# Kernel tuning notes

Measured on AMD Instinct MI355X. Metric: run time of the kernel, lower is better.

The kernel has to match this reference:

```python
import jax, jax.numpy as jnp
import numpy as np

B, T, D, H = 2, 2048, 2048, 32
HD = D // H
# quantization scales (constructor-time attributes in the original repo)
A_PROJ = 3e-4   # q/k/v proj alpha (W8A8B8O8Linear)
A_QK = 2e-5     # qk_bmm alpha (BMM_S8T_S8N_F32T)
A_PV = 1e-2     # pv_bmm alpha (BMM_S8T_S8N_S8T)
A_OUT = 1e-4    # out_proj alpha (W8A8BFP32OFP32Linear)


def _i8(key, shape):
    return jax.random.randint(key, shape, -128, 128, dtype=jnp.int32).astype(jnp.int8)


def setup_inputs() -> dict:
    key = jax.random.key(0)
    ks = jax.random.split(key, 10)
    hidden_states = _i8(ks[0], (B, T, D))
    # causal mask, 0 on/below diagonal, large negative above
    causal = jnp.triu(jnp.full((T, T), -1e9, dtype=jnp.float32), k=1)
    attention_mask = jnp.broadcast_to(causal, (B, 1, T, T))
    return {
        "hidden_states": hidden_states,
        "attention_mask": attention_mask,
        "Wq": _i8(ks[1], (D, D)), "bq": _i8(ks[2], (D,)),
        "Wk": _i8(ks[3], (D, D)), "bk": _i8(ks[4], (D,)),
        "Wv": _i8(ks[5], (D, D)), "bv": _i8(ks[6], (D,)),
        "Wo": _i8(ks[7], (D, D)),
        "bo": jax.random.normal(ks[8], (D,), dtype=jnp.float32),
    }


def _w8a8b8o8(x_i8, W_i8, b_i8, alpha):
    # int8 GEMM -> int32 accum; epilogue: alpha*acc + bias, saturate to int8
    acc = jnp.einsum('btk,nk->btn', x_i8.astype(jnp.int32), W_i8.astype(jnp.int32))
    y = alpha * acc.astype(jnp.float32) + b_i8.astype(jnp.float32)
    return jnp.clip(jnp.round(y), -128, 127).astype(jnp.int8)


def reference(hidden_states, attention_mask, Wq, bq, Wk, bk, Wv, bv, Wo, bo):
    # q/k/v projections: int8 in, int8 out
    q = _w8a8b8o8(hidden_states, Wq, bq, A_PROJ)
    k = _w8a8b8o8(hidden_states, Wk, bk, A_PROJ)
    v = _w8a8b8o8(hidden_states, Wv, bv, A_PROJ)

    def shape(x):  # [B,T,D] -> [B,H,T,HD]
        return x.reshape(B, T, H, HD).transpose(0, 2, 1, 3)

    qh, kh, vh = shape(q), shape(k), shape(v)

    # qk_bmm (BMM_S8T_S8N_F32T): fp32 = alpha * int8 q @ k^T
    attn = A_QK * jnp.einsum('bhtd,bhsd->bhts',
                             qh.astype(jnp.int32), kh.astype(jnp.int32)).astype(jnp.float32)
    attn = attn + attention_mask  # [B,1,T,T] broadcasts over heads
    attn = jnp.maximum(attn, jnp.finfo(jnp.float32).min)
    probs = jax.nn.softmax(attn, axis=-1)

    # quantize probs: p.mul_(127).round_() -> int8
    p_i8 = jnp.clip(jnp.round(probs * 127.0), -128, 127).astype(jnp.int8)

    # pv_bmm (BMM_S8T_S8N_S8T): int8 out = sat(round(alpha * p @ v))
    pv = jnp.einsum('bhts,bhsd->bhtd', p_i8.astype(jnp.int32), vh.astype(jnp.int32))
    attn_out_i8 = jnp.clip(jnp.round(A_PV * pv.astype(jnp.float32)), -128, 127).astype(jnp.int8)

    # [B,H,T,HD] -> [B,T,D]
    attn_out = attn_out_i8.transpose(0, 2, 1, 3).reshape(B, T, D)

    # out_proj (W8A8BFP32OFP32Linear): fp32 = alpha*(x@W^T) + fp32 bias
    acc = jnp.einsum('btk,nk->btn', attn_out.astype(jnp.int32), Wo.astype(jnp.int32))
    out = A_OUT * acc.astype(jnp.float32) + bo
    return out
```

## Files before the change

### kernel.cpp

```cpp
#include <hip/hip_runtime.h>
#include <cstdint>

#define A_PROJ 3e-4f
#define A_QK   2e-5f
#define A_PV   1e-2f
#define A_OUT  1e-4f

#define NB 2
#define NT 2048
#define ND 2048
#define NH 32
#define NHD 64
#define NM (NB*NT)

typedef int v4i __attribute__((ext_vector_type(4)));

__device__ __forceinline__ int8_t sat8(float y) {
  float r = rintf(y);
  r = fminf(fmaxf(r, -128.f), 127.f);
  return (int8_t)(int)r;
}

__device__ __forceinline__ float exp2_fast(float x) {
  return __builtin_amdgcn_exp2f(x);
}

__device__ __forceinline__ void gl2lds16(const int8_t* g, int8_t* l) {
  __builtin_amdgcn_global_load_lds(
      (const __attribute__((address_space(1))) void*)g,
      (__attribute__((address_space(3))) void*)l, 16, 0, 0);
}

#define NWW (ND*ND/4)
__global__ void pack_all(const int* __restrict__ X,
                         const int* __restrict__ W0, const int* __restrict__ W1,
                         const int* __restrict__ W2, const int* __restrict__ W3,
                         int8_t* __restrict__ dX, int8_t* __restrict__ dW0,
                         int8_t* __restrict__ dW1, int8_t* __restrict__ dW2,
                         int8_t* __restrict__ dW3) {
  int i = blockIdx.x * blockDim.x + threadIdx.x;
  const int nx = NM*ND/4;
  const int* src; int8_t* dst; int off;
  if (i < nx) { src = X; dst = dX; off = i; }
  else {
    int j = i - nx;
    int r = j >> 20;
    off = j & (NWW - 1);
    src = (r == 0) ? W0 : (r == 1) ? W1 : (r == 2) ? W2 : W3;
    dst = (r == 0) ? dW0 : (r == 1) ? dW1 : (r == 2) ? dW2 : dW3;
  }
  int4 v = ((const int4*)src)[off];
  uint32_t p = (uint32_t)(v.x & 255) | ((uint32_t)(v.y & 255) << 8) |
               ((uint32_t)(v.z & 255) << 16) | ((uint32_t)(v.w & 255) << 24);
  ((uint32_t*)dst)[off] = p;
}

__global__ __launch_bounds__(256) void gemm_qkv(
    const int8_t* __restrict__ X,
    const int8_t* __restrict__ Wq, const int8_t* __restrict__ Wk, const int8_t* __restrict__ Wv,
    const int* __restrict__ bq, const int* __restrict__ bk, const int* __restrict__ bv,
    int8_t* __restrict__ Qh, int8_t* __restrict__ Kh, int8_t* __restrict__ Vt)
{
  __shared__ __align__(16) int8_t As[2][128][64];
  __shared__ __align__(16) int8_t Bs[2][128][64];
  const int z = blockIdx.z;
  const int8_t* W  = (z == 0) ? Wq : ((z == 1) ? Wk : Wv);
  const int* bias  = (z == 0) ? bq : ((z == 1) ? bk : bv);
  const int m0 = blockIdx.x * 128, n0 = blockIdx.y * 128;
  const int tid = threadIdx.x, lane = tid & 63, wave = tid >> 6;
  const int wm = wave >> 1, wn = wave & 1;
  const int l15 = lane & 15, quad = lane >> 4;

  const int srow = lane >> 2;
  const int scol = (((lane & 3) ^ ((lane >> 3) & 3)) * 16);
  const int rqcol = (quad ^ ((l15 >> 1) & 3)) * 16;

  v4i acc[4][4];
  const v4i vzero = {0, 0, 0, 0};
  #pragma unroll
  for (int i = 0; i < 4; ++i)
    #pragma unroll
    for (int j = 0; j < 4; ++j) acc[i][j] = vzero;

  for (int k0 = 0; k0 < ND; k0 += 128) {
    #pragma unroll
    for (int j = 0; j < 8; ++j) {
      int slot = j * 4 + wave;
      int sl = slot & 15;
      int hh = sl >> 3, rblk = sl & 7;
      int row = rblk * 16 + srow;
      if (slot < 16) {
        gl2lds16(&X[(size_t)(m0 + row) * ND + k0 + hh * 64 + scol], &As[hh][rblk * 16][0]);
      } else {
        gl2lds16(&W[(size_t)(n0 + row) * ND + k0 + hh * 64 + scol], &Bs[hh][rblk * 16][0]);
      }
    }
    __syncthreads();
    #pragma unroll
    for (int hh = 0; hh < 2; ++hh) {
      v4i a[4], b[4];
      #pragma unroll
      for (int mt = 0; mt < 4; ++mt) a[mt] = *(const v4i*)&As[hh][wm*64 + mt*16 + l15][rqcol];
      #pragma unroll
      for (int nt = 0; nt < 4; ++nt) b[nt] = *(const v4i*)&Bs[hh][wn*64 + nt*16 + l15][rqcol];
      #pragma unroll
      for (int mt = 0; mt < 4; ++mt)
        #pragma unroll
        for (int nt = 0; nt < 4; ++nt)
          acc[mt][nt] = __builtin_amdgcn_mfma_i32_16x16x64_i8(a[mt], b[nt], acc[mt][nt], 0, 0, 0);
    }
    __syncthreads();
  }

  float bf[4];
  #pragma unroll
  for (int nt = 0; nt < 4; ++nt) bf[nt] = (float)bias[n0 + wn*64 + nt*16 + l15];

  if (z == 2) {
    #pragma unroll
    for (int mt = 0; mt < 4; ++mt)
      #pragma unroll
      for (int nt = 0; nt < 4; ++nt) {
        int tbase = (m0 + wm*64 + mt*16 + quad*4) & (NT - 1);
        int bb = (m0 + wm*64) >> 11;
        int n = n0 + wn*64 + nt*16 + l15;
        int hh = n >> 6, hd = n & (NHD - 1);
        uint32_t pk = 0;
        #pragma unroll
        for (int r = 0; r < 4; ++r) {
          uint32_t q = (uint32_t)(uint8_t)sat8(A_PROJ * (float)acc[mt][nt][r] + bf[nt]);
          pk |= q << (8 * r);
        }
        size_t bh = (size_t)bb * NH + hh;
        *(uint32_t*)&Vt[(bh * NHD + hd) * NT + tbase] = pk;
      }
  } else {
    int8_t* O = (z == 0) ? Qh : Kh;
    #pragma unroll
    for (int mt = 0; mt < 4; ++mt)
      #pragma unroll
      for (int nt = 0; nt < 4; ++nt)
        #pragma unroll
        for (int r = 0; r < 4; ++r) {
          int m = m0 + wm*64 + mt*16 + quad*4 + r;
          int n = n0 + wn*64 + nt*16 + l15;
          int8_t q = sat8(A_PROJ * (float)acc[mt][nt][r] + bf[nt]);
          int bb = m >> 11, t = m & (NT - 1);
          int hh = n >> 6, hd = n & (NHD - 1);
          size_t bh = (size_t)bb * NH + hh;
          O[(bh * NT + t) * NHD + hd] = q;
        }
  }
}

__global__ __launch_bounds__(256) void attn_fused(
    const int8_t* __restrict__ Qh, const int8_t* __restrict__ Kh, const int8_t* __restrict__ Vt,
    int8_t* __restrict__ AO)
{
  __shared__ __align__(16) int8_t Ks[128][64];
  __shared__ __align__(16) int8_t Vs[64][128];
  __shared__ __align__(16) uint32_t Ps32[4][16][36];

  const int bx = blockIdx.x;
  const int bh = blockIdx.y;
  const int tid = threadIdx.x, lane = tid & 63, wave = tid >> 6;
  const int l15 = lane & 15, quad = lane >> 4;
  const v4i vzero = {0, 0, 0, 0};
  const float MAGIC = 12582912.0f;
  const float C2 = 2.8853900817779268e-05f;

  const int8_t* Qp = Qh + (size_t)bh * NT * NHD;
  const int8_t* Kp = Kh + (size_t)bh * NT * NHD;
  const int8_t* Vp = Vt + (size_t)bh * NHD * NT;
  const int bb = bh >> 5, hhead = bh & (NH - 1);

  const int kst_row = lane >> 2;
  const int kst_col = (((lane & 3) ^ ((lane >> 3) & 3)) * 16);
  const int vst_row = lane >> 3;
  const int vst_col = (((lane & 7) ^ ((lane >> 3) & 7)) * 16);
  const int kfcol = (quad ^ ((l15 >> 1) & 3)) * 16;

  for (int half = 0; half < 2; ++half) {
    const int xq = half ? (31 - bx) : bx;
    const int t0 = xq * 64;
    const int sd = xq >> 1;
    const int tme = t0 + wave * 16 + l15;

    v4i qf = *(const v4i*)&Qp[(size_t)(t0 + wave * 16 + l15) * NHD + quad * 16];

    float lsum = 0.f;
    for (int st = 0; st <= sd; ++st) {
      const int s0 = st * 128;
      #pragma unroll
      for (int j = 0; j < 2; ++j)
        gl2lds16(&Kp[(size_t)(s0 + j*64 + wave*16 + kst_row) * NHD + kst_col],
                 &Ks[j*64 + wave*16][0]);
      __syncthreads();
      v4i kf[8];
      #pragma unroll
      for (int mt = 0; mt < 8; ++mt) kf[mt] = *(const v4i*)&Ks[mt*16 + l15][kfcol];
      if (st < sd) {
        #pragma unroll
        for (int mt = 0; mt < 8; ++mt) {
          v4i sa = __builtin_amdgcn_mfma_i32_16x16x64_i8(kf[mt], qf, vzero, 0, 0, 0);
          #pragma unroll
          for (int r = 0; r < 4; ++r) lsum += exp2_fast(C2 * (float)sa[r]);
        }
      } else {
        #pragma unroll
        for (int mt = 0; mt < 8; ++mt) {
          v4i sa = __builtin_amdgcn_mfma_i32_16x16x64_i8(kf[mt], qf, vzero, 0, 0, 0);
          const int sbase = s0 + mt*16 + quad*4;
          #pragma unroll
          for (int r = 0; r < 4; ++r) {
            float e = exp2_fast(C2 * (float)sa[r]);
            lsum += (sbase + r <= tme) ? e : 0.f;
          }
        }
      }
      __syncthreads();
    }
    {
      lsum += __shfl_xor(lsum, 16, 64);
      lsum += __shfl_xor(lsum, 32, 64);
    }
    const float linv = 127.0f / lsum;

    v4i accv[4];
    #pragma unroll
    for (int j = 0; j < 4; ++j) accv[j] = vzero;

    for (int st = 0; st <= sd; ++st) {
      const int s0 = st * 128;
      #pragma unroll
      for (int j = 0; j < 2; ++j)
        gl2lds16(&Kp[(size_t)(s0 + j*64 + wave*16 + kst_row) * NHD + kst_col],
                 &Ks[j*64 + wave*16][0]);
      #pragma unroll
      for (int j = 0; j < 2; ++j)
        gl2lds16(&Vp[(size_t)(j*32 + wave*8 + vst_row) * NT + s0 + vst_col],
                 &Vs[j*32 + wave*8][0]);
      __syncthreads();
      v4i kf[8];
      #pragma unroll
      for (int mt = 0; mt < 8; ++mt) kf[mt] = *(const v4i*)&Ks[mt*16 + l15][kfcol];

      if (st < sd) {
        #pragma unroll
        for (int mt = 0; mt < 8; ++mt) {
          v4i sa = __builtin_amdgcn_mfma_i32_16x16x64_i8(kf[mt], qf, vzero, 0, 0, 0);
          uint32_t pk = 0;
          #pragma unroll
          for (int r = 0; r < 4; ++r) {
            float e = exp2_fast(C2 * (float)sa[r]);
            float f = fmaf(e, linv, MAGIC);
            pk |= (__float_as_uint(f) & 0xFFu) << (8 * r);
          }
          Ps32[wave][l15][mt*4 + quad] = pk;
        }
      } else {
        #pragma unroll
        for (int mt = 0; mt < 8; ++mt) {
          v4i sa = __builtin_amdgcn_mfma_i32_16x16x64_i8(kf[mt], qf, vzero, 0, 0, 0);
          uint32_t pk = 0;
          const int sbase = s0 + mt*16 + quad*4;
          #pragma unroll
          for (int r = 0; r < 4; ++r) {
            float e = (sbase + r <= tme) ? exp2_fast(C2 * (float)sa[r]) : 0.f;
            float f = fmaf(e, linv, MAGIC);
            pk |= (__float_as_uint(f) & 0xFFu) << (8 * r);
          }
          Ps32[wave][l15][mt*4 + quad] = pk;
        }
      }
      #pragma unroll
      for (int ks = 0; ks < 2; ++ks) {
        v4i ap = *(const v4i*)&Ps32[wave][l15][ks*16 + quad*4];
        #pragma unroll
        for (int nt2 = 0; nt2 < 4; ++nt2) {
          v4i bv = *(const v4i*)&Vs[nt2*16 + l15][(((ks*4 + quad) ^ (l15 & 7)) * 16)];
          accv[nt2] = __builtin_amdgcn_mfma_i32_16x16x64_i8(ap, bv, accv[nt2], 0, 0, 0);
        }
      }
      __syncthreads();
    }

    #pragma unroll
    for (int nt2 = 0; nt2 < 4; ++nt2)
      #pragma unroll
      for (int r = 0; r < 4; ++r) {
        int t = t0 + wave*16 + quad*4 + r;
        int d = nt2*16 + l15;
        AO[((size_t)bb * NT + t) * ND + hhead * NHD + d] = sat8(A_PV * (float)accv[nt2][r]);
      }
  }
}

__global__ __launch_bounds__(256) void gemm_out(
    const int8_t* __restrict__ X, const int8_t* __restrict__ W,
    const float* __restrict__ bo, float* __restrict__ out)
{
  __shared__ __align__(16) int8_t As[2][128][64];
  __shared__ __align__(16) int8_t Bs[2][128][64];
  const int m0 = blockIdx.x * 128, n0 = blockIdx.y * 128;
  const int tid = threadIdx.x, lane = tid & 63, wave = tid >> 6;
  const int wm = wave >> 1, wn = wave & 1;
  const int l15 = lane & 15, quad = lane >> 4;
  const int srow = lane >> 2;
  const int scol = (((lane & 3) ^ ((lane >> 3) & 3)) * 16);
  const int rqcol = (quad ^ ((l15 >> 1) & 3)) * 16;

  v4i acc[4][4];
  const v4i vzero = {0, 0, 0, 0};
  #pragma unroll
  for (int i = 0; i < 4; ++i)
    #pragma unroll
    for (int j = 0; j < 4; ++j) acc[i][j] = vzero;

  for (int k0 = 0; k0 < ND; k0 += 128) {
    #pragma unroll
    for (int j = 0; j < 8; ++j) {
      int slot = j * 4 + wave;
      int sl = slot & 15;
      int hh = sl >> 3, rblk = sl & 7;
      int row = rblk * 16 + srow;
      if (slot < 16) {
        gl2lds16(&X[(size_t)(m0 + row) * ND + k0 + hh * 64 + scol], &As[hh][rblk * 16][0]);
      } else {
        gl2lds16(&W[(size_t)(n0 + row) * ND + k0 + hh * 64 + scol], &Bs[hh][rblk * 16][0]);
      }
    }
    __syncthreads();
    #pragma unroll
    for (int hh = 0; hh < 2; ++hh) {
      v4i a[4], b[4];
      #pragma unroll
      for (int mt = 0; mt < 4; ++mt) a[mt] = *(const v4i*)&As[hh][wm*64 + mt*16 + l15][rqcol];
      #pragma unroll
      for (int nt = 0; nt < 4; ++nt) b[nt] = *(const v4i*)&Bs[hh][wn*64 + nt*16 + l15][rqcol];
      #pragma unroll
      for (int mt = 0; mt < 4; ++mt)
        #pragma unroll
        for (int nt = 0; nt < 4; ++nt)
          acc[mt][nt] = __builtin_amdgcn_mfma_i32_16x16x64_i8(a[mt], b[nt], acc[mt][nt], 0, 0, 0);
    }
    __syncthreads();
  }

  float bf[4];
  #pragma unroll
  for (int nt = 0; nt < 4; ++nt) bf[nt] = bo[n0 + wn*64 + nt*16 + l15];

  #pragma unroll
  for (int mt = 0; mt < 4; ++mt)
    #pragma unroll
    for (int nt = 0; nt < 4; ++nt)
      #pragma unroll
      for (int r = 0; r < 4; ++r) {
        int m = m0 + wm*64 + mt*16 + quad*4 + r;
        int n = n0 + wn*64 + nt*16 + l15;
        out[(size_t)m * ND + n] = A_OUT * (float)acc[mt][nt][r] + bf[nt];
      }
}

extern "C" void kernel_launch(void* const* d_in, const int* in_sizes, int n_in,
                              void* d_out, int out_size, void* d_ws, size_t ws_size,
                              hipStream_t stream)
{
  const int*   hs  = (const int*)d_in[0];
  const int*   Wq  = (const int*)d_in[2];
  const int*   bq  = (const int*)d_in[3];
  const int*   Wk  = (const int*)d_in[4];
  const int*   bkb = (const int*)d_in[5];
  const int*   Wv  = (const int*)d_in[6];
  const int*   bvb = (const int*)d_in[7];
  const int*   Wo  = (const int*)d_in[8];
  const float* bo  = (const float*)d_in[9];
  float* out = (float*)d_out;

  char* ws = (char*)d_ws;
  const size_t SZ_X = (size_t)NM * ND;
  const size_t SZ_W = (size_t)ND * ND;
  const size_t SZ_H = (size_t)NB * NH * NT * NHD;
  int8_t* Xp  = (int8_t*)ws;
  int8_t* Wqp = (int8_t*)(ws + SZ_X);
  int8_t* Wkp = Wqp + SZ_W;
  int8_t* Wvp = Wkp + SZ_W;
  int8_t* Wop = Wvp + SZ_W;
  int8_t* Qh  = Wop + SZ_W;
  int8_t* Kh  = Qh + SZ_H;
  int8_t* Vt  = Kh + SZ_H;
  int8_t* AO  = Xp;

  const int ntot = (int)(SZ_X/4 + 4 * (SZ_W/4));
  pack_all<<<(ntot + 255) / 256, 256, 0, stream>>>(hs, Wq, Wk, Wv, Wo,
                                                   Xp, Wqp, Wkp, Wvp, Wop);

  gemm_qkv<<<dim3(NM/128, ND/128, 3), 256, 0, stream>>>(Xp, Wqp, Wkp, Wvp, bq, bkb, bvb, Qh, Kh, Vt);
  attn_fused<<<dim3(16, NB*NH), 256, 0, stream>>>(Qh, Kh, Vt, AO);
  gemm_out<<<dim3(NM/128, ND/128), 256, 0, stream>>>(AO, Wop, bo, out);
}
```

Measured before the change: 328.7 us.

## Double-buffer LDS loads in GEMMs and attention, skip masked causal tiles

Both int8 GEMMs move from single-stage 128-wide K tiles to a double-buffered 64-wide K pipeline, so the next tile's global-to-LDS load overlaps the current MFMA work. The attention kernel double-buffers its K tiles the same way, reads V fragments straight from global memory into registers instead of staging them in LDS, and on the diagonal tile skips MFMA/exp work for 16-row subtiles that are fully masked. It also splits the row-sum accumulator into four partial sums and packs the probability bytes with perm instructions. The costs are extra LDS for the second buffer, uncoalesced direct global V loads, and a smaller K step per barrier in the GEMMs.

```diff
diff --git a/kernel.cpp b/kernel.cpp
--- a/kernel.cpp
+++ b/kernel.cpp
@@ -75,6 +75,11 @@
   const int scol = (((lane & 3) ^ ((lane >> 3) & 3)) * 16);
   const int rqcol = (quad ^ ((l15 >> 1) & 3)) * 16;
 
+  const int8_t* Xs0 = X + (size_t)(m0 + wave * 32 + srow) * ND + scol;
+  const int8_t* Xs1 = X + (size_t)(m0 + wave * 32 + 16 + srow) * ND + scol;
+  const int8_t* Ws0 = W + (size_t)(n0 + wave * 32 + srow) * ND + scol;
+  const int8_t* Ws1 = W + (size_t)(n0 + wave * 32 + 16 + srow) * ND + scol;
+
   v4i acc[4][4];
   const v4i vzero = {0, 0, 0, 0};
   #pragma unroll
@@ -82,33 +87,31 @@
     #pragma unroll
     for (int j = 0; j < 4; ++j) acc[i][j] = vzero;
 
-  for (int k0 = 0; k0 < ND; k0 += 128) {
-    #pragma unroll
-    for (int j = 0; j < 8; ++j) {
-      int slot = j * 4 + wave;
-      int sl = slot & 15;
-      int hh = sl >> 3, rblk = sl & 7;
-      int row = rblk * 16 + srow;
-      if (slot < 16) {
-        gl2lds16(&X[(size_t)(m0 + row) * ND + k0 + hh * 64 + scol], &As[hh][rblk * 16][0]);
-      } else {
-        gl2lds16(&W[(size_t)(n0 + row) * ND + k0 + hh * 64 + scol], &Bs[hh][rblk * 16][0]);
-      }
+  gl2lds16(Xs0, &As[0][wave * 32][0]);
+  gl2lds16(Xs1, &As[0][wave * 32 + 16][0]);
+  gl2lds16(Ws0, &Bs[0][wave * 32][0]);
+  gl2lds16(Ws1, &Bs[0][wave * 32 + 16][0]);
+  __syncthreads();
+
+  for (int h = 0; h < 32; ++h) {
+    const int buf = h & 1;
+    if (h < 31) {
+      const int off = (h + 1) * 64;
+      gl2lds16(Xs0 + off, &As[buf ^ 1][wave * 32][0]);
+      gl2lds16(Xs1 + off, &As[buf ^ 1][wave * 32 + 16][0]);
+      gl2lds16(Ws0 + off, &Bs[buf ^ 1][wave * 32][0]);
+      gl2lds16(Ws1 + off, &Bs[buf ^ 1][wave * 32 + 16][0]);
     }
-    __syncthreads();
-    #pragma unroll
-    for (int hh = 0; hh < 2; ++hh) {
-      v4i a[4], b[4];
-      #pragma unroll
-      for (int mt = 0; mt < 4; ++mt) a[mt] = *(const v4i*)&As[hh][wm*64 + mt*16 + l15][rqcol];
-      #pragma unroll
-      for (int nt = 0; nt < 4; ++nt) b[nt] = *(const v4i*)&Bs[hh][wn*64 + nt*16 + l15][rqcol];
-      #pragma unroll
-      for (int mt = 0; mt < 4; ++mt)
-        #pragma unroll
-        for (int nt = 0; nt < 4; ++nt)
-          acc[mt][nt] = __builtin_amdgcn_mfma_i32_16x16x64_i8(a[mt], b[nt], acc[mt][nt], 0, 0, 0);
-    }
+    v4i a[4], b[4];
+    #pragma unroll
+    for (int mt = 0; mt < 4; ++mt) a[mt] = *(const v4i*)&As[buf][wm*64 + mt*16 + l15][rqcol];
+    #pragma unroll
+    for (int nt = 0; nt < 4; ++nt) b[nt] = *(const v4i*)&Bs[buf][wn*64 + nt*16 + l15][rqcol];
+    #pragma unroll
+    for (int mt = 0; mt < 4; ++mt)
+      #pragma unroll
+      for (int nt = 0; nt < 4; ++nt)
+        acc[mt][nt] = __builtin_amdgcn_mfma_i32_16x16x64_i8(a[mt], b[nt], acc[mt][nt], 0, 0, 0);
     __syncthreads();
   }
 
@@ -157,8 +160,7 @@
     const int8_t* __restrict__ Qh, const int8_t* __restrict__ Kh, const int8_t* __restrict__ Vt,
     int8_t* __restrict__ AO)
 {
-  __shared__ __align__(16) int8_t Ks[128][64];
-  __shared__ __align__(16) int8_t Vs[64][128];
+  __shared__ __align__(16) int8_t Ks[2][128][64];
   __shared__ __align__(16) uint32_t Ps32[4][16][36];
 
   const int bx = blockIdx.x;
@@ -176,8 +178,6 @@
 
   const int kst_row = lane >> 2;
   const int kst_col = (((lane & 3) ^ ((lane >> 3) & 3)) * 16);
-  const int vst_row = lane >> 3;
-  const int vst_col = (((lane & 7) ^ ((lane >> 3) & 7)) * 16);
   const int kfcol = (quad ^ ((l15 >> 1) & 3)) * 16;
 
   for (int half = 0; half < 2; ++half) {
@@ -185,102 +185,123 @@
     const int t0 = xq * 64;
     const int sd = xq >> 1;
     const int tme = t0 + wave * 16 + l15;
+    const int mtd = ((xq & 1) << 2) + wave;
 
     v4i qf = *(const v4i*)&Qp[(size_t)(t0 + wave * 16 + l15) * NHD + quad * 16];
 
-    float lsum = 0.f;
+    gl2lds16(&Kp[(size_t)(wave*16 + kst_row) * NHD + kst_col], &Ks[0][wave*16][0]);
+    gl2lds16(&Kp[(size_t)(64 + wave*16 + kst_row) * NHD + kst_col], &Ks[0][64 + wave*16][0]);
+    __syncthreads();
+
+    float lac[4] = {0.f, 0.f, 0.f, 0.f};
     for (int st = 0; st <= sd; ++st) {
-      const int s0 = st * 128;
-      #pragma unroll
-      for (int j = 0; j < 2; ++j)
-        gl2lds16(&Kp[(size_t)(s0 + j*64 + wave*16 + kst_row) * NHD + kst_col],
-                 &Ks[j*64 + wave*16][0]);
-      __syncthreads();
-      v4i kf[8];
-      #pragma unroll
-      for (int mt = 0; mt < 8; ++mt) kf[mt] = *(const v4i*)&Ks[mt*16 + l15][kfcol];
+      const int buf = st & 1;
       if (st < sd) {
+        const size_t s1 = (size_t)(st + 1) * 128;
+        gl2lds16(&Kp[(s1 + wave*16 + kst_row) * NHD + kst_col], &Ks[buf^1][wave*16][0]);
+        gl2lds16(&Kp[(s1 + 64 + wave*16 + kst_row) * NHD + kst_col], &Ks[buf^1][64 + wave*16][0]);
+      }
+      if (st < sd) {
         #pragma unroll
         for (int mt = 0; mt < 8; ++mt) {
-          v4i sa = __builtin_amdgcn_mfma_i32_16x16x64_i8(kf[mt], qf, vzero, 0, 0, 0);
+          v4i kf = *(const v4i*)&Ks[buf][mt*16 + l15][kfcol];
+          v4i sa = __builtin_amdgcn_mfma_i32_16x16x64_i8(kf, qf, vzero, 0, 0, 0);
           #pragma unroll
-          for (int r = 0; r < 4; ++r) lsum += exp2_fast(C2 * (float)sa[r]);
+          for (int r = 0; r < 4; ++r) lac[r] += exp2_fast(C2 * (float)sa[r]);
         }
       } else {
-        #pragma unroll
-        for (int mt = 0; mt < 8; ++mt) {
-          v4i sa = __builtin_amdgcn_mfma_i32_16x16x64_i8(kf[mt], qf, vzero, 0, 0, 0);
-          const int sbase = s0 + mt*16 + quad*4;
-          #pragma unroll
-          for (int r = 0; r < 4; ++r) {
-            float e = exp2_fast(C2 * (float)sa[r]);
-            lsum += (sbase + r <= tme) ? e : 0.f;
+        const int s0 = st * 128;
+        for (int mt = 0; mt <= mtd; ++mt) {
+          v4i kf = *(const v4i*)&Ks[buf][mt*16 + l15][kfcol];
+          v4i sa = __builtin_amdgcn_mfma_i32_16x16x64_i8(kf, qf, vzero, 0, 0, 0);
+          if (mt < mtd) {
+            #pragma unroll
+            for (int r = 0; r < 4; ++r) lac[r] += exp2_fast(C2 * (float)sa[r]);
+          } else {
+            const int sbase = s0 + mt*16 + quad*4;
+            #pragma unroll
+            for (int r = 0; r < 4; ++r) {
+              float e = exp2_fast(C2 * (float)sa[r]);
+              lac[r] += (sbase + r <= tme) ? e : 0.f;
+            }
           }
         }
       }
       __syncthreads();
     }
-    {
-      lsum += __shfl_xor(lsum, 16, 64);
-      lsum += __shfl_xor(lsum, 32, 64);
-    }
+    float lsum = (lac[0] + lac[1]) + (lac[2] + lac[3]);
+    lsum += __shfl_xor(lsum, 16, 64);
+    lsum += __shfl_xor(lsum, 32, 64);
     const float linv = 127.0f / lsum;
 
+    gl2lds16(&Kp[(size_t)(wave*16 + kst_row) * NHD + kst_col], &Ks[0][wave*16][0]);
+    gl2lds16(&Kp[(size_t)(64 + wave*16 + kst_row) * NHD + kst_col], &Ks[0][64 + wave*16][0]);
+    __syncthreads();
+
     v4i accv[4];
     #pragma unroll
     for (int j = 0; j < 4; ++j) accv[j] = vzero;
 
     for (int st = 0; st <= sd; ++st) {
+      const int buf = st & 1;
       const int s0 = st * 128;
-      #pragma unroll
-      for (int j = 0; j < 2; ++j)
-        gl2lds16(&Kp[(size_t)(s0 + j*64 + wave*16 + kst_row) * NHD + kst_col],
-                 &Ks[j*64 + wave*16][0]);
-      #pragma unroll
-      for (int j = 0; j < 2; ++j)
-        gl2lds16(&Vp[(size_t)(j*32 + wave*8 + vst_row) * NT + s0 + vst_col],
-                 &Vs[j*32 + wave*8][0]);
-      __syncthreads();
-      v4i kf[8];
-      #pragma unroll
-      for (int mt = 0; mt < 8; ++mt) kf[mt] = *(const v4i*)&Ks[mt*16 + l15][kfcol];
-
       if (st < sd) {
+        const size_t s1 = (size_t)(st + 1) * 128;
+        gl2lds16(&Kp[(s1 + wave*16 + kst_row) * NHD + kst_col], &Ks[buf^1][wave*16][0]);
+        gl2lds16(&Kp[(s1 + 64 + wave*16 + kst_row) * NHD + kst_col], &Ks[buf^1][64 + wave*16][0]);
+      }
+      v4i bv[8];
+      #pragma unroll
+      for (int ks = 0; ks < 2; ++ks)
+        #pragma unroll
+        for (int nt = 0; nt < 4; ++nt)
+          bv[ks*4 + nt] = *(const v4i*)&Vp[(size_t)(nt*16 + l15) * NT + s0 + ks*64 + quad*16];
+
+      if (st < sd) {
         #pragma unroll
         for (int mt = 0; mt < 8; ++mt) {
-          v4i sa = __builtin_amdgcn_mfma_i32_16x16x64_i8(kf[mt], qf, vzero, 0, 0, 0);
-          uint32_t pk = 0;
-          #pragma unroll
-          for (int r = 0; r < 4; ++r) {
-            float e = exp2_fast(C2 * (float)sa[r]);
-            float f = fmaf(e, linv, MAGIC);
-            pk |= (__float_as_uint(f) & 0xFFu) << (8 * r);
+          v4i kf = *(const v4i*)&Ks[buf][mt*16 + l15][kfcol];
+          v4i sa = __builtin_amdgcn_mfma_i32_16x16x64_i8(kf, qf, vzero, 0, 0, 0);
+          uint32_t f0 = __float_as_uint(fmaf(exp2_fast(C2 * (float)sa[0]), linv, MAGIC));
+          uint32_t f1 = __float_as_uint(fmaf(exp2_fast(C2 * (float)sa[1]), linv, MAGIC));
+          uint32_t f2 = __float_as_uint(fmaf(exp2_fast(C2 * (float)sa[2]), linv, MAGIC));
+          uint32_t f3 = __float_as_uint(fmaf(exp2_fast(C2 * (float)sa[3]), linv, MAGIC));
+          uint32_t lo = __builtin_amdgcn_perm(f1, f0, 0x00000400u);
+          uint32_t hi = __builtin_amdgcn_perm(f3, f2, 0x00000400u);
+          Ps32[wave][l15][mt*4 + quad] = __builtin_amdgcn_perm(hi, lo, 0x05040100u);
+        }
+      } else {
+        for (int mt = 0; mt <= mtd; ++mt) {
+          v4i kf = *(const v4i*)&Ks[buf][mt*16 + l15][kfcol];
+          v4i sa = __builtin_amdgcn_mfma_i32_16x16x64_i8(kf, qf, vzero, 0, 0, 0);
+          float e0, e1, e2, e3;
+          if (mt < mtd) {
+            e0 = exp2_fast(C2 * (float)sa[0]); e1 = exp2_fast(C2 * (float)sa[1]);
+            e2 = exp2_fast(C2 * (float)sa[2]); e3 = exp2_fast(C2 * (float)sa[3]);
+          } else {
+            const int sbase = s0 + mt*16 + quad*4;
+            e0 = (sbase + 0 <= tme) ? exp2_fast(C2 * (float)sa[0]) : 0.f;
+            e1 = (sbase + 1 <= tme) ? exp2_fast(C2 * (float)sa[1]) : 0.f;
+            e2 = (sbase + 2 <= tme) ? exp2_fast(C2 * (float)sa[2]) : 0.f;
+            e3 = (sbase + 3 <= tme) ? exp2_fast(C2 * (float)sa[3]) : 0.f;
           }
-          Ps32[wave][l15][mt*4 + quad] = pk;
-        }
-      } else {
-        #pragma unroll
-        for (int mt = 0; mt < 8; ++mt) {
-          v4i sa = __builtin_amdgcn_mfma_i32_16x16x64_i8(kf[mt], qf, vzero, 0, 0, 0);
-          uint32_t pk = 0;
-          const int sbase = s0 + mt*16 + quad*4;
-          #pragma unroll
-          for (int r = 0; r < 4; ++r) {
-            float e = (sbase + r <= tme) ? exp2_fast(C2 * (float)sa[r]) : 0.f;
-            float f = fmaf(e, linv, MAGIC);
-            pk |= (__float_as_uint(f) & 0xFFu) << (8 * r);
-          }
-          Ps32[wave][l15][mt*4 + quad] = pk;
-        }
+          uint32_t f0 = __float_as_uint(fmaf(e0, linv, MAGIC));
+          uint32_t f1 = __float_as_uint(fmaf(e1, linv, MAGIC));
+          uint32_t f2 = __float_as_uint(fmaf(e2, linv, MAGIC));
+          uint32_t f3 = __float_as_uint(fmaf(e3, linv, MAGIC));
+          uint32_t lo = __builtin_amdgcn_perm(f1, f0, 0x00000400u);
+          uint32_t hi = __builtin_amdgcn_perm(f3, f2, 0x00000400u);
+          Ps32[wave][l15][mt*4 + quad] = __builtin_amdgcn_perm(hi, lo, 0x05040100u);
+        }
+        for (int mt = mtd + 1; mt < 8; ++mt)
+          Ps32[wave][l15][mt*4 + quad] = 0u;
       }
       #pragma unroll
       for (int ks = 0; ks < 2; ++ks) {
         v4i ap = *(const v4i*)&Ps32[wave][l15][ks*16 + quad*4];
         #pragma unroll
-        for (int nt2 = 0; nt2 < 4; ++nt2) {
-          v4i bv = *(const v4i*)&Vs[nt2*16 + l15][(((ks*4 + quad) ^ (l15 & 7)) * 16)];
-          accv[nt2] = __builtin_amdgcn_mfma_i32_16x16x64_i8(ap, bv, accv[nt2], 0, 0, 0);
-        }
+        for (int nt2 = 0; nt2 < 4; ++nt2)
+          accv[nt2] = __builtin_amdgcn_mfma_i32_16x16x64_i8(ap, bv[ks*4 + nt2], accv[nt2], 0, 0, 0);
       }
       __syncthreads();
     }
@@ -310,6 +331,11 @@
   const int scol = (((lane & 3) ^ ((lane >> 3) & 3)) * 16);
   const int rqcol = (quad ^ ((l15 >> 1) & 3)) * 16;
 
+  const int8_t* Xs0 = X + (size_t)(m0 + wave * 32 + srow) * ND + scol;
+  const int8_t* Xs1 = X + (size_t)(m0 + wave * 32 + 16 + srow) * ND + scol;
+  const int8_t* Ws0 = W + (size_t)(n0 + wave * 32 + srow) * ND + scol;
+  const int8_t* Ws1 = W + (size_t)(n0 + wave * 32 + 16 + srow) * ND + scol;
+
   v4i acc[4][4];
   const v4i vzero = {0, 0, 0, 0};
   #pragma unroll
@@ -317,33 +343,31 @@
     #pragma unroll
     for (int j = 0; j < 4; ++j) acc[i][j] = vzero;
 
-  for (int k0 = 0; k0 < ND; k0 += 128) {
-    #pragma unroll
-    for (int j = 0; j < 8; ++j) {
-      int slot = j * 4 + wave;
-      int sl = slot & 15;
-      int hh = sl >> 3, rblk = sl & 7;
-      int row = rblk * 16 + srow;
-      if (slot < 16) {
-        gl2lds16(&X[(size_t)(m0 + row) * ND + k0 + hh * 64 + scol], &As[hh][rblk * 16][0]);
-      } else {
-        gl2lds16(&W[(size_t)(n0 + row) * ND + k0 + hh * 64 + scol], &Bs[hh][rblk * 16][0]);
-      }
+  gl2lds16(Xs0, &As[0][wave * 32][0]);
+  gl2lds16(Xs1, &As[0][wave * 32 + 16][0]);
+  gl2lds16(Ws0, &Bs[0][wave * 32][0]);
+  gl2lds16(Ws1, &Bs[0][wave * 32 + 16][0]);
+  __syncthreads();
+
+  for (int h = 0; h < 32; ++h) {
+    const int buf = h & 1;
+    if (h < 31) {
+      const int off = (h + 1) * 64;
+      gl2lds16(Xs0 + off, &As[buf ^ 1][wave * 32][0]);
+      gl2lds16(Xs1 + off, &As[buf ^ 1][wave * 32 + 16][0]);
+      gl2lds16(Ws0 + off, &Bs[buf ^ 1][wave * 32][0]);
+      gl2lds16(Ws1 + off, &Bs[buf ^ 1][wave * 32 + 16][0]);
     }
-    __syncthreads();
-    #pragma unroll
-    for (int hh = 0; hh < 2; ++hh) {
-      v4i a[4], b[4];
-      #pragma unroll
-      for (int mt = 0; mt < 4; ++mt) a[mt] = *(const v4i*)&As[hh][wm*64 + mt*16 + l15][rqcol];
-      #pragma unroll
-      for (int nt = 0; nt < 4; ++nt) b[nt] = *(const v4i*)&Bs[hh][wn*64 + nt*16 + l15][rqcol];
-      #pragma unroll
-      for (int mt = 0; mt < 4; ++mt)
-        #pragma unroll
-        for (int nt = 0; nt < 4; ++nt)
-          acc[mt][nt] = __builtin_amdgcn_mfma_i32_16x16x64_i8(a[mt], b[nt], acc[mt][nt], 0, 0, 0);
-    }
+    v4i a[4], b[4];
+    #pragma unroll
+    for (int mt = 0; mt < 4; ++mt) a[mt] = *(const v4i*)&As[buf][wm*64 + mt*16 + l15][rqcol];
+    #pragma unroll
+    for (int nt = 0; nt < 4; ++nt) b[nt] = *(const v4i*)&Bs[buf][wn*64 + nt*16 + l15][rqcol];
+    #pragma unroll
+    for (int mt = 0; mt < 4; ++mt)
+      #pragma unroll
+      for (int nt = 0; nt < 4; ++nt)
+        acc[mt][nt] = __builtin_amdgcn_mfma_i32_16x16x64_i8(a[mt], b[nt], acc[mt][nt], 0, 0, 0);
     __syncthreads();
   }
 
```

Result: slower. 363.9 us (+10.7%).
